# Optimization experiments

Hardware: AMD Instinct MI355X
Metric: run time of the kernel (lower is better)

Reference implementation:

```python
import jax, jax.numpy as jnp
import numpy as np

B, S, H = 4, 4096, 1024
F = 2048          # expert_intermediate_size
E = 8             # num_experts (== num_local_experts, no expert parallelism)
TOPK = 2
INIT_STD = 0.02


def setup_inputs() -> dict:
    key = jax.random.key(0)
    k_hs, k_w, k_e, k_w1, k_w2 = jax.random.split(key, 5)
    hidden_states = jax.random.normal(k_hs, (B, S, H), dtype=jnp.float32)
    expert_weights = jax.random.uniform(k_w, (B * S, TOPK), dtype=jnp.float32)
    top_experts = jax.random.randint(k_e, (B * S, TOPK), 0, E).astype(jnp.int64)
    w1 = INIT_STD * jax.random.normal(k_w1, (E, H, F), dtype=jnp.float32)
    w2 = INIT_STD * jax.random.normal(k_w2, (E, F, H), dtype=jnp.float32)
    b1 = jnp.zeros((E, F), dtype=jnp.float32)
    b2 = jnp.zeros((E, H), dtype=jnp.float32)
    return {"hidden_states": hidden_states, "expert_weights": expert_weights,
            "top_experts": top_experts, "w1": w1, "b1": b1, "w2": w2, "b2": b2}


def reference(hidden_states, expert_weights, top_experts, w1, b1, w2, b2):
    # Equivalent math to megablocks-style gather -> grouped GEMM -> weighted scatter,
    # expressed as masked per-expert GEMMs (sort/permute is a pure reordering and
    # cancels out in the scatter-with-weights combine).
    b, s, h = hidden_states.shape
    x = hidden_states.reshape(-1, h)                       # [T, H]
    T = x.shape[0]
    topk = top_experts.shape[-1]
    fe = top_experts.reshape(-1)                           # [T*topk] routed expert ids
    fw = expert_weights.reshape(-1)                        # [T*topk] routing weights
    xr = jnp.repeat(x, topk, axis=0)                       # [T*topk, H] (gather w/ topk replication)
    out = jnp.zeros_like(xr)
    n_experts = w1.shape[0]
    for e in range(n_experts):                             # small fixed expert loop
        he = jax.nn.gelu(xr @ w1[e] + b1[e], approximate=False) @ w2[e] + b2[e]
        out = out + jnp.where((fe == e)[:, None], he, 0.0)
    # scatter back with routing weights: weighted sum over topk per token
    y = (fw[:, None] * out).reshape(T, topk, h).sum(axis=1)
    return y.reshape(b, s, h)
```

## Files before the change

### kernel.cpp

```cpp
#include <hip/hip_runtime.h>
#include <hip/hip_bf16.h>
#include <math.h>

#define TOKENS 16384
#define HD 1024
#define FD 2048
#define NEXP 8
#define RP_MAX (264 * 128)
#define MAX_MT 264
#define NTN1 16
#define NTN2 8

#define NB_CONV 2048
#define NB_W1   1024
#define NB_W2   1024
#define NB_PREP (NB_CONV + NB_W1 + NB_W2 + 1)

typedef __bf16 bf16x8 __attribute__((ext_vector_type(8)));
typedef float f32x4 __attribute__((ext_vector_type(4)));
typedef unsigned short u16;
typedef unsigned int u32;
typedef unsigned long long u64;

__device__ __forceinline__ u16 f2bf(float f) {
    union { float f; u32 u; } v; v.f = f;
    return (u16)((v.u + 0x7FFFu + ((v.u >> 16) & 1u)) >> 16);
}

__device__ __forceinline__ u32 pk_bf16(float lo, float hi) {
    u32 p;
    asm("v_cvt_pk_bf16_f32 %0, %1, %2" : "=v"(p) : "v"(lo), "v"(hi));
    return p;
}

__device__ __forceinline__ float gelu_f(float v) {
    float u = __builtin_fmaf(0.044715f * v * v, v, v);
    float ez = __builtin_amdgcn_exp2f(-2.302208f * u);
    return v * __builtin_amdgcn_rcpf(1.0f + ez);
}

#define GLOAD16(g, l) __builtin_amdgcn_global_load_lds( \
    (const __attribute__((address_space(1))) u32*)(g),  \
    (__attribute__((address_space(3))) u32*)(l), 16, 0, 0)

__global__ __launch_bounds__(1024) void mega_prep(
    const float* __restrict__ x, u16* __restrict__ xb,
    const float* __restrict__ w1, u16* __restrict__ w1t,
    const float* __restrict__ w2, u16* __restrict__ w2t,
    const int* __restrict__ te,
    int* sorted_rid, int* inv, int* tileE, int* tileRow,
    int* numTiles, int* padcum)
{
    __shared__ __align__(16) char ldsT[32768];
    __shared__ int cntS[NEXP], offsS[NEXP], fillS[NEXP], padS[NEXP], ntS;
    int b = blockIdx.x;
    int tid = threadIdx.x;

    if (b < NB_CONV) {
        int i = b * 1024 + tid;
        const float4* xv = (const float4*)x;
        float4 a = xv[i * 2], c = xv[i * 2 + 1];
        union { u16 s[8]; uint4 v; } o;
        o.s[0] = f2bf(a.x); o.s[1] = f2bf(a.y); o.s[2] = f2bf(a.z); o.s[3] = f2bf(a.w);
        o.s[4] = f2bf(c.x); o.s[5] = f2bf(c.y); o.s[6] = f2bf(c.z); o.s[7] = f2bf(c.w);
        *(uint4*)(xb + (size_t)i * 8) = o.v;
        return;
    }
    if (b < NB_CONV + NB_W1 + NB_W2) {
        const float* src; u16* dst; int K, N, n0, k0, e;
        if (b < NB_CONV + NB_W1) {
            int bb = b - NB_CONV;
            e = bb >> 7; int r = bb & 127;
            n0 = (r & 15) * 128; k0 = (r >> 4) * 128;
            K = HD; N = FD; src = w1; dst = w1t;
        } else {
            int bb = b - NB_CONV - NB_W1;
            e = bb >> 7; int r = bb & 127;
            n0 = (r & 7) * 128; k0 = (r >> 3) * 128;
            K = FD; N = HD; src = w2; dst = w2t;
        }
        const float* s = src + (size_t)e * K * N + (size_t)k0 * N + n0;
        u16* d = dst + (size_t)e * N * K + (size_t)n0 * K + k0;
        int tx = tid & 31, ty = tid >> 5;
        #pragma unroll
        for (int p = 0; p < 4; p++) {
            int k = p * 32 + ty;
            float4 v = *(const float4*)(s + (size_t)k * N + tx * 4);
            union { u16 q[4]; u64 u; } o;
            o.q[0] = f2bf(v.x); o.q[1] = f2bf(v.y); o.q[2] = f2bf(v.z); o.q[3] = f2bf(v.w);
            int phys = tx ^ (k & 31);
            *(u64*)(ldsT + k * 256 + phys * 8) = o.u;
        }
        __syncthreads();
        int tx2 = tid & 15, ty2 = tid >> 4;
        #pragma unroll
        for (int p = 0; p < 2; p++) {
            int n = p * 64 + ty2;
            union { u16 q[8]; uint4 u; } o;
            #pragma unroll
            for (int j = 0; j < 8; j++) {
                int k = tx2 * 8 + j;
                int phys = (n >> 2) ^ (k & 31);
                o.q[j] = *(const u16*)(ldsT + k * 256 + phys * 8 + (n & 3) * 2);
            }
            *(uint4*)(d + (size_t)n * K + tx2 * 8) = o.u;
        }
        return;
    }

    int lane = tid & 63;
    if (tid < NEXP) cntS[tid] = 0;
    __syncthreads();
    int h[NEXP] = {0, 0, 0, 0, 0, 0, 0, 0};
    for (int j = tid; j < TOKENS * 2; j += 1024) {
        int v = te[j];
        #pragma unroll
        for (int e = 0; e < NEXP; e++) h[e] += (v == e);
    }
    #pragma unroll
    for (int e = 0; e < NEXP; e++) {
        int s = h[e];
        #pragma unroll
        for (int o = 32; o > 0; o >>= 1) s += __shfl_down(s, o, 64);
        if (lane == 0 && s) atomicAdd(&cntS[e], s);
    }
    __syncthreads();
    if (tid == 0) {
        int o = 0, t = 0, pc = 0;
        for (int e = 0; e < NEXP; e++) {
            offsS[e] = o; fillS[e] = 0;
            int pad = o - pc;
            padS[e] = pad; padcum[e] = pad;
            int c = cntS[e];
            int nt = (c + 127) >> 7;
            for (int i = 0; i < nt; i++) { tileE[t] = e; tileRow[t] = o + i * 128; t++; }
            o += nt * 128; pc += c;
        }
        ntS = t;
        *numTiles = t;
    }
    __syncthreads();
    int tot = ntS * 128;
    for (int i = tid; i < tot; i += 1024) sorted_rid[i] = -1;
    __syncthreads();
    for (int j = tid; j < TOKENS * 2; j += 1024) {
        int v = te[j];
        int base = 0;
        #pragma unroll
        for (int e = 0; e < NEXP; e++) {
            unsigned long long m = __ballot(v == e);
            if (m) {
                int ldr = (int)__builtin_ctzll(m);
                int bb = 0;
                if (lane == ldr) bb = atomicAdd(&fillS[e], __popcll(m));
                bb = __shfl(bb, ldr, 64);
                if (v == e) base = bb + (int)__popcll(m & ((1ull << lane) - 1ull));
            }
        }
        int p = offsS[v] + base;
        sorted_rid[p] = j;
        inv[j] = p - padS[v];
    }
}



__global__ __launch_bounds__(256, 2) void gemm1_kernel(
    const u16* __restrict__ Xb, const u16* __restrict__ W1t,
    const float* __restrict__ b1, const int* __restrict__ sorted_rid,
    const int* __restrict__ tileE, const int* __restrict__ tileRow,
    const int* __restrict__ numTiles, u16* __restrict__ Hact)
{
    int bid = blockIdx.x;
    int xcd = bid & 7, slot = bid >> 3;
    int mt = xcd + (slot / NTN1) * 8;
    int n0 = (slot % NTN1) * 128;
    if (mt >= *numTiles) return;
    int e = tileE[mt];
    int row0 = tileRow[mt];

    __shared__ __align__(16) u16 As[128 * 64];
    __shared__ __align__(16) u16 Bs[128 * 64];

    int tid = threadIdx.x;
    int wave = tid >> 6, lane = tid & 63;
    int laneR = lane & 15, kgrp = lane >> 4;

    const u16* gA[4]; const u16* gB[4];
    #pragma unroll
    for (int i = 0; i < 4; i++) {
        int c = i * 256 + tid;
        int r = c >> 3, kc = c & 7;
        int kcs = kc ^ (r & 7);
        int rid = sorted_rid[row0 + r];
        int tok = rid < 0 ? 0 : (rid >> 1);
        gA[i] = Xb + (size_t)tok * HD + kcs * 8;
        gB[i] = W1t + ((size_t)e * FD + (n0 + r)) * HD + kcs * 8;
    }
    char* AsB = (char*)As; char* BsB = (char*)Bs;

    f32x4 acc[4][4] = {};

    int wr = wave >> 1, wc = wave & 1;
    int off0 = ((kgrp ^ (lane & 7)) << 4);
    int off1 = off0 ^ 64;
    const char* Abase = AsB + (wr * 64 + laneR) * 128;
    const char* Bbase = BsB + (wc * 64 + laneR) * 128;

    for (int kt = 0; kt < HD / 64; kt++) {
        #pragma unroll
        for (int i = 0; i < 4; i++)
            GLOAD16(gA[i], AsB + i * 4096 + wave * 1024);
        #pragma unroll
        for (int i = 0; i < 4; i++)
            GLOAD16(gB[i], BsB + i * 4096 + wave * 1024);
        #pragma unroll
        for (int i = 0; i < 4; i++) { gA[i] += 64; gB[i] += 64; }
        __syncthreads();
        #pragma unroll
        for (int kk = 0; kk < 2; kk++) {
            int off = kk ? off1 : off0;
            bf16x8 a[4], b[4];
            #pragma unroll
            for (int m = 0; m < 4; m++) a[m] = *(const bf16x8*)(Abase + m * 2048 + off);
            #pragma unroll
            for (int n = 0; n < 4; n++) b[n] = *(const bf16x8*)(Bbase + n * 2048 + off);
            #pragma unroll
            for (int m = 0; m < 4; m++)
                #pragma unroll
                for (int n = 0; n < 4; n++)
                    acc[m][n] = __builtin_amdgcn_mfma_f32_16x16x32_bf16(b[n], a[m], acc[m][n], 0, 0, 0);
        }
        __syncthreads();
    }

    const float* b1e = b1 + e * FD + n0;
    #pragma unroll
    for (int mf = 0; mf < 4; mf++) {
        int grow = row0 + wr * 64 + mf * 16 + laneR;
        u16* hrow = Hact + (size_t)grow * FD + n0;
        #pragma unroll
        for (int nf = 0; nf < 4; nf++) {
            int c = wc * 64 + nf * 16 + kgrp * 4;
            float4 bb = *(const float4*)(b1e + c);
            float g0 = gelu_f(acc[mf][nf][0] + bb.x);
            float g1 = gelu_f(acc[mf][nf][1] + bb.y);
            float g2 = gelu_f(acc[mf][nf][2] + bb.z);
            float g3 = gelu_f(acc[mf][nf][3] + bb.w);
            uint2 p = make_uint2(pk_bf16(g0, g1), pk_bf16(g2, g3));
            *(uint2*)(hrow + c) = p;
        }
    }
}


__global__ __launch_bounds__(256, 2) void gemm2_kernel(
    const u16* __restrict__ Hact, const u16* __restrict__ W2t,
    const float* __restrict__ b2, const int* __restrict__ sorted_rid,
    const int* __restrict__ padcum,
    const int* __restrict__ tileE, const int* __restrict__ tileRow,
    const int* __restrict__ numTiles, u16* __restrict__ Out2)
{
    int bid = blockIdx.x;
    int xcd = bid & 7, slot = bid >> 3;
    int mt = xcd + (slot / NTN2) * 8;
    int n0 = (slot % NTN2) * 128;
    if (mt >= *numTiles) return;
    int e = tileE[mt];
    int row0 = tileRow[mt];

    __shared__ __align__(16) u16 As[128 * 64];
    __shared__ __align__(16) u16 Bs[128 * 64];

    int tid = threadIdx.x;
    int wave = tid >> 6, lane = tid & 63;
    int laneR = lane & 15, kgrp = lane >> 4;

    const u16* gA[4]; const u16* gB[4];
    #pragma unroll
    for (int i = 0; i < 4; i++) {
        int c = i * 256 + tid;
        int r = c >> 3, kc = c & 7;
        int kcs = kc ^ (r & 7);
        gA[i] = Hact + (size_t)(row0 + r) * FD + kcs * 8;
        gB[i] = W2t + ((size_t)e * HD + (n0 + r)) * FD + kcs * 8;
    }
    char* AsB = (char*)As; char* BsB = (char*)Bs;

    f32x4 acc[4][4] = {};

    int wr = wave >> 1, wc = wave & 1;
    int off0 = ((kgrp ^ (lane & 7)) << 4);
    int off1 = off0 ^ 64;
    const char* Abase = AsB + (wr * 64 + laneR) * 128;
    const char* Bbase = BsB + (wc * 64 + laneR) * 128;

    for (int kt = 0; kt < FD / 64; kt++) {
        #pragma unroll
        for (int i = 0; i < 4; i++)
            GLOAD16(gA[i], AsB + i * 4096 + wave * 1024);
        #pragma unroll
        for (int i = 0; i < 4; i++)
            GLOAD16(gB[i], BsB + i * 4096 + wave * 1024);
        #pragma unroll
        for (int i = 0; i < 4; i++) { gA[i] += 64; gB[i] += 64; }
        __syncthreads();
        #pragma unroll
        for (int kk = 0; kk < 2; kk++) {
            int off = kk ? off1 : off0;
            bf16x8 a[4], b[4];
            #pragma unroll
            for (int m = 0; m < 4; m++) a[m] = *(const bf16x8*)(Abase + m * 2048 + off);
            #pragma unroll
            for (int n = 0; n < 4; n++) b[n] = *(const bf16x8*)(Bbase + n * 2048 + off);
            #pragma unroll
            for (int m = 0; m < 4; m++)
                #pragma unroll
                for (int n = 0; n < 4; n++)
                    acc[m][n] = __builtin_amdgcn_mfma_f32_16x16x32_bf16(b[n], a[m], acc[m][n], 0, 0, 0);
        }
        __syncthreads();
    }

    const float* b2e = b2 + e * HD + n0;
    int pc = padcum[e];
    #pragma unroll
    for (int mf = 0; mf < 4; mf++) {
        int rr = row0 + wr * 64 + mf * 16 + laneR;
        int rid = sorted_rid[rr];
        if (rid < 0) continue;
        u16* orow = Out2 + (size_t)(rr - pc) * HD + n0;
        #pragma unroll
        for (int nf = 0; nf < 4; nf++) {
            int c = wc * 64 + nf * 16 + kgrp * 4;
            float4 bb = *(const float4*)(b2e + c);
            float v0 = acc[mf][nf][0] + bb.x;
            float v1 = acc[mf][nf][1] + bb.y;
            float v2 = acc[mf][nf][2] + bb.z;
            float v3 = acc[mf][nf][3] + bb.w;
            uint2 p = make_uint2(pk_bf16(v0, v1), pk_bf16(v2, v3));
            *(uint2*)(orow + c) = p;
        }
    }
}


__global__ void combine_kernel(const u16* __restrict__ Out2, const int* __restrict__ inv,
                               const float* __restrict__ ew, float* __restrict__ y) {
    int i = blockIdx.x * blockDim.x + threadIdx.x;
    int tok = i >> 7;
    int c0 = (i & 127) << 3;
    int s0 = inv[2 * tok], s1 = inv[2 * tok + 1];
    float w0 = ew[2 * tok], w1 = ew[2 * tok + 1];
    union { uint4 v; u16 s[8]; } a, b;
    a.v = *(const uint4*)(Out2 + (size_t)s0 * HD + c0);
    b.v = *(const uint4*)(Out2 + (size_t)s1 * HD + c0);
    float out[8];
    #pragma unroll
    for (int j = 0; j < 8; j++) {
        union { u32 u; float f; } fa, fb;
        fa.u = (u32)a.s[j] << 16;
        fb.u = (u32)b.s[j] << 16;
        out[j] = w0 * fa.f + w1 * fb.f;
    }
    float4* yp = (float4*)(y + (size_t)tok * HD + c0);
    yp[0] = *(const float4*)&out[0];
    yp[1] = *(const float4*)&out[4];
}


extern "C" void kernel_launch(void* const* d_in, const int* in_sizes, int n_in,
                              void* d_out, int out_size, void* d_ws, size_t ws_size,
                              hipStream_t stream) {
    const float* x  = (const float*)d_in[0];
    const float* ew = (const float*)d_in[1];
    const int*   te = (const int*)d_in[2];
    const float* w1 = (const float*)d_in[3];
    const float* b1 = (const float*)d_in[4];
    const float* w2 = (const float*)d_in[5];
    const float* b2 = (const float*)d_in[6];
    float* y = (float*)d_out;

    char* ws = (char*)d_ws;
    u16* Xb   = (u16*)(ws);
    u16* W1t  = (u16*)(ws + 33554432);
    u16* Out2 = (u16*)(ws);
    u16* W2t  = (u16*)(ws + 67108864);
    u16* Hact = (u16*)(ws + 100663296);
    char* ip  = ws + 239075328;
    int* numTiles = (int*)(ip);
    int* padcum   = (int*)(ip + 64);
    int* tileE    = (int*)(ip + 128);
    int* tileRow  = (int*)(ip + 2048);
    int* sorted   = (int*)(ip + 4096);
    int* inv      = (int*)(ip + 139264);

    mega_prep<<<NB_PREP, 1024, 0, stream>>>(
        x, Xb, w1, W1t, w2, W2t, te, sorted, inv, tileE, tileRow, numTiles, padcum);

    gemm1_kernel<<<MAX_MT * NTN1, 256, 0, stream>>>(
        Xb, W1t, b1, sorted, tileE, tileRow, numTiles, Hact);

    gemm2_kernel<<<MAX_MT * NTN2, 256, 0, stream>>>(
        Hact, W2t, b2, sorted, padcum, tileE, tileRow, numTiles, Out2);

    combine_kernel<<<(TOKENS * 128) / 256, 256, 0, stream>>>(Out2, inv, ew, y);
}
```

Before: 445.5 us.

## Move W2 conversion into gemm1 tail blocks and start routing block first

The fp32-to-bf16 transpose of w2 moves out of the prep kernel and into 1024 extra blocks appended to the gemm1 grid, where it can fill idle slots while the GEMM runs. The single-block routing/sort work moves to block 0 of the prep kernel so it is scheduled first rather than last, shortening the prep kernel's critical tail. The transpose blocks use 256 threads instead of 1024, and gemm1's shared buffers become one array so the transpose can reuse them. The risk is that the extra blocks compete with gemm1 tiles for CU occupancy and memory bandwidth.

After: 446.4 us. Within noise of the previous version (+0.2%).

```diff
diff --git a/kernel.cpp b/kernel.cpp
--- a/kernel.cpp
+++ b/kernel.cpp
@@ -13,8 +13,10 @@
 
 #define NB_CONV 2048
 #define NB_W1   1024
-#define NB_W2   1024
-#define NB_PREP (NB_CONV + NB_W1 + NB_W2 + 1)
+#define NB_PREP (1 + NB_CONV + NB_W1)
+
+#define G1_BLOCKS (MAX_MT * NTN1)
+#define NB_W2     1024
 
 typedef __bf16 bf16x8 __attribute__((ext_vector_type(8)));
 typedef float f32x4 __attribute__((ext_vector_type(4)));
@@ -46,7 +48,6 @@
 __global__ __launch_bounds__(1024) void mega_prep(
     const float* __restrict__ x, u16* __restrict__ xb,
     const float* __restrict__ w1, u16* __restrict__ w1t,
-    const float* __restrict__ w2, u16* __restrict__ w2t,
     const int* __restrict__ te,
     int* sorted_rid, int* inv, int* tileE, int* tileRow,
     int* numTiles, int* padcum)
@@ -56,8 +57,64 @@
     int b = blockIdx.x;
     int tid = threadIdx.x;
 
-    if (b < NB_CONV) {
-        int i = b * 1024 + tid;
+    if (b == 0) {
+        int lane = tid & 63;
+        if (tid < NEXP) cntS[tid] = 0;
+        __syncthreads();
+        int h[NEXP] = {0, 0, 0, 0, 0, 0, 0, 0};
+        for (int j = tid; j < TOKENS * 2; j += 1024) {
+            int v = te[j];
+            #pragma unroll
+            for (int e = 0; e < NEXP; e++) h[e] += (v == e);
+        }
+        #pragma unroll
+        for (int e = 0; e < NEXP; e++) {
+            int s = h[e];
+            #pragma unroll
+            for (int o = 32; o > 0; o >>= 1) s += __shfl_down(s, o, 64);
+            if (lane == 0 && s) atomicAdd(&cntS[e], s);
+        }
+        __syncthreads();
+        if (tid == 0) {
+            int o = 0, t = 0, pc = 0;
+            for (int e = 0; e < NEXP; e++) {
+                offsS[e] = o; fillS[e] = 0;
+                int pad = o - pc;
+                padS[e] = pad; padcum[e] = pad;
+                int c = cntS[e];
+                int nt = (c + 127) >> 7;
+                for (int i = 0; i < nt; i++) { tileE[t] = e; tileRow[t] = o + i * 128; t++; }
+                o += nt * 128; pc += c;
+            }
+            ntS = t;
+            *numTiles = t;
+        }
+        __syncthreads();
+        int tot = ntS * 128;
+        for (int i = tid; i < tot; i += 1024) sorted_rid[i] = -1;
+        __syncthreads();
+        for (int j = tid; j < TOKENS * 2; j += 1024) {
+            int v = te[j];
+            int base = 0;
+            #pragma unroll
+            for (int e = 0; e < NEXP; e++) {
+                unsigned long long m = __ballot(v == e);
+                if (m) {
+                    int ldr = (int)__builtin_ctzll(m);
+                    int bb = 0;
+                    if (lane == ldr) bb = atomicAdd(&fillS[e], __popcll(m));
+                    bb = __shfl(bb, ldr, 64);
+                    if (v == e) base = bb + (int)__popcll(m & ((1ull << lane) - 1ull));
+                }
+            }
+            int p = offsS[v] + base;
+            sorted_rid[p] = j;
+            inv[j] = p - padS[v];
+        }
+        return;
+    }
+    if (b <= NB_CONV) {
+        int i = (b - 1) * 1024 + tid;
         const float4* xv = (const float4*)x;
         float4 a = xv[i * 2], c = xv[i * 2 + 1];
         union { u16 s[8]; uint4 v; } o;
@@ -66,21 +123,13 @@
         *(uint4*)(xb + (size_t)i * 8) = o.v;
         return;
     }
-    if (b < NB_CONV + NB_W1 + NB_W2) {
-        const float* src; u16* dst; int K, N, n0, k0, e;
-        if (b < NB_CONV + NB_W1) {
-            int bb = b - NB_CONV;
-            e = bb >> 7; int r = bb & 127;
-            n0 = (r & 15) * 128; k0 = (r >> 4) * 128;
-            K = HD; N = FD; src = w1; dst = w1t;
-        } else {
-            int bb = b - NB_CONV - NB_W1;
-            e = bb >> 7; int r = bb & 127;
-            n0 = (r & 7) * 128; k0 = (r >> 3) * 128;
-            K = FD; N = HD; src = w2; dst = w2t;
-        }
-        const float* s = src + (size_t)e * K * N + (size_t)k0 * N + n0;
-        u16* d = dst + (size_t)e * N * K + (size_t)n0 * K + k0;
+    {
+        int bb = b - 1 - NB_CONV;
+        int e = bb >> 7; int r = bb & 127;
+        int n0 = (r & 15) * 128, k0 = (r >> 4) * 128;
+        const int K = HD, N = FD;
+        const float* s = w1 + (size_t)e * K * N + (size_t)k0 * N + n0;
+        u16* d = w1t + (size_t)e * N * K + (size_t)n0 * K + k0;
         int tx = tid & 31, ty = tid >> 5;
         #pragma unroll
         for (int p = 0; p < 4; p++) {
@@ -105,61 +154,6 @@
             }
             *(uint4*)(d + (size_t)n * K + tx2 * 8) = o.u;
         }
-        return;
-    }
-
-    int lane = tid & 63;
-    if (tid < NEXP) cntS[tid] = 0;
-    __syncthreads();
-    int h[NEXP] = {0, 0, 0, 0, 0, 0, 0, 0};
-    for (int j = tid; j < TOKENS * 2; j += 1024) {
-        int v = te[j];
-        #pragma unroll
-        for (int e = 0; e < NEXP; e++) h[e] += (v == e);
-    }
-    #pragma unroll
-    for (int e = 0; e < NEXP; e++) {
-        int s = h[e];
-        #pragma unroll
-        for (int o = 32; o > 0; o >>= 1) s += __shfl_down(s, o, 64);
-        if (lane == 0 && s) atomicAdd(&cntS[e], s);
-    }
-    __syncthreads();
-    if (tid == 0) {
-        int o = 0, t = 0, pc = 0;
-        for (int e = 0; e < NEXP; e++) {
-            offsS[e] = o; fillS[e] = 0;
-            int pad = o - pc;
-            padS[e] = pad; padcum[e] = pad;
-            int c = cntS[e];
-            int nt = (c + 127) >> 7;
-            for (int i = 0; i < nt; i++) { tileE[t] = e; tileRow[t] = o + i * 128; t++; }
-            o += nt * 128; pc += c;
-        }
-        ntS = t;
-        *numTiles = t;
-    }
-    __syncthreads();
-    int tot = ntS * 128;
-    for (int i = tid; i < tot; i += 1024) sorted_rid[i] = -1;
-    __syncthreads();
-    for (int j = tid; j < TOKENS * 2; j += 1024) {
-        int v = te[j];
-        int base = 0;
-        #pragma unroll
-        for (int e = 0; e < NEXP; e++) {
-            unsigned long long m = __ballot(v == e);
-            if (m) {
-                int ldr = (int)__builtin_ctzll(m);
-                int bb = 0;
-                if (lane == ldr) bb = atomicAdd(&fillS[e], __popcll(m));
-                bb = __shfl(bb, ldr, 64);
-                if (v == e) base = bb + (int)__popcll(m & ((1ull << lane) - 1ull));
-            }
-        }
-        int p = offsS[v] + base;
-        sorted_rid[p] = j;
-        inv[j] = p - padS[v];
     }
 }
 
@@ -169,9 +163,48 @@
     const u16* __restrict__ Xb, const u16* __restrict__ W1t,
     const float* __restrict__ b1, const int* __restrict__ sorted_rid,
     const int* __restrict__ tileE, const int* __restrict__ tileRow,
-    const int* __restrict__ numTiles, u16* __restrict__ Hact)
+    const int* __restrict__ numTiles, u16* __restrict__ Hact,
+    const float* __restrict__ w2, u16* __restrict__ w2t)
 {
+    __shared__ __align__(16) u16 SMEM[2 * 128 * 64];
+    int tid = threadIdx.x;
     int bid = blockIdx.x;
+
+    if (bid >= G1_BLOCKS) {
+        char* ldsT = (char*)SMEM;
+        int bb = bid - G1_BLOCKS;
+        int e = bb >> 7; int r = bb & 127;
+        int n0 = (r & 7) * 128, k0 = (r >> 3) * 128;
+        const int K = FD, N = HD;
+        const float* s = w2 + (size_t)e * K * N + (size_t)k0 * N + n0;
+        u16* d = w2t + (size_t)e * N * K + (size_t)n0 * K + k0;
+        #pragma unroll
+        for (int p = 0; p < 16; p++) {
+            int idx = p * 256 + tid;
+            int k = idx >> 5, tx = idx & 31;
+            float4 v = *(const float4*)(s + (size_t)k * N + tx * 4);
+            union { u16 q[4]; u64 u; } o;
+            o.q[0] = f2bf(v.x); o.q[1] = f2bf(v.y); o.q[2] = f2bf(v.z); o.q[3] = f2bf(v.w);
+            int phys = tx ^ (k & 31);
+            *(u64*)(ldsT + k * 256 + phys * 8) = o.u;
+        }
+        __syncthreads();
+        #pragma unroll
+        for (int p = 0; p < 8; p++) {
+            int idx = p * 256 + tid;
+            int n = idx >> 4, tx2 = idx & 15;
+            union { u16 q[8]; uint4 u; } o;
+            #pragma unroll
+            for (int j = 0; j < 8; j++) {
+                int k = tx2 * 8 + j;
+                int phys = (n >> 2) ^ (k & 31);
+                o.q[j] = *(const u16*)(ldsT + k * 256 + phys * 8 + (n & 3) * 2);
+            }
+            *(uint4*)(d + (size_t)n * K + tx2 * 8) = o.u;
+        }
+        return;
+    }
+
     int xcd = bid & 7, slot = bid >> 3;
     int mt = xcd + (slot / NTN1) * 8;
     int n0 = (slot % NTN1) * 128;
@@ -179,10 +212,6 @@
     int e = tileE[mt];
     int row0 = tileRow[mt];
 
-    __shared__ __align__(16) u16 As[128 * 64];
-    __shared__ __align__(16) u16 Bs[128 * 64];
-
-    int tid = threadIdx.x;
     int wave = tid >> 6, lane = tid & 63;
     int laneR = lane & 15, kgrp = lane >> 4;
 
@@ -197,7 +226,8 @@
         gA[i] = Xb + (size_t)tok * HD + kcs * 8;
         gB[i] = W1t + ((size_t)e * FD + (n0 + r)) * HD + kcs * 8;
     }
-    char* AsB = (char*)As; char* BsB = (char*)Bs;
+    char* AsB = (char*)SMEM;
+    char* BsB = (char*)(SMEM + 128 * 64);
 
     f32x4 acc[4][4] = {};
 
@@ -396,10 +426,10 @@
     int* inv      = (int*)(ip + 139264);
 
     mega_prep<<<NB_PREP, 1024, 0, stream>>>(
-        x, Xb, w1, W1t, w2, W2t, te, sorted, inv, tileE, tileRow, numTiles, padcum);
-
-    gemm1_kernel<<<MAX_MT * NTN1, 256, 0, stream>>>(
-        Xb, W1t, b1, sorted, tileE, tileRow, numTiles, Hact);
+        x, Xb, w1, W1t, te, sorted, inv, tileE, tileRow, numTiles, padcum);
+
+    gemm1_kernel<<<G1_BLOCKS + NB_W2, 256, 0, stream>>>(
+        Xb, W1t, b1, sorted, tileE, tileRow, numTiles, Hact, w2, W2t);
 
     gemm2_kernel<<<MAX_MT * NTN2, 256, 0, stream>>>(
         Hact, W2t, b2, sorted, padcum, tileE, tileRow, numTiles, Out2);
```

## Move routing block first in prep and group GEMM tiles for L2 reuse

Applied to the files above, without the earlier changes.

The serial routing/sort block in the prep kernel moves from the last block index to block 0, so it is scheduled first and overlaps with the conversion blocks instead of trailing them. The GEMM block-to-tile mapping now groups four M tiles together across the N tiles within each XCD, aiming for better weight/activation reuse in cache. Grid sizes are recomputed as 8*9*4*NTN, which gives 288 M tiles against the earlier 264 and so adds some blocks that exit early.

New measurement: 429.0 us. 1.04x faster.

```diff
diff --git a/kernel.cpp b/kernel.cpp
--- a/kernel.cpp
+++ b/kernel.cpp
@@ -8,13 +8,17 @@
 #define NEXP 8
 #define RP_MAX (264 * 128)
 #define MAX_MT 264
+#define MTL_MAX 33
+#define QG 9
 #define NTN1 16
 #define NTN2 8
+#define G1_BLOCKS (8 * QG * 4 * NTN1)
+#define G2_BLOCKS (8 * QG * 4 * NTN2)
 
 #define NB_CONV 2048
 #define NB_W1   1024
 #define NB_W2   1024
-#define NB_PREP (NB_CONV + NB_W1 + NB_W2 + 1)
+#define NB_PREP (1 + NB_CONV + NB_W1 + NB_W2)
 
 typedef __bf16 bf16x8 __attribute__((ext_vector_type(8)));
 typedef float f32x4 __attribute__((ext_vector_type(4)));
@@ -56,8 +60,64 @@
     int b = blockIdx.x;
     int tid = threadIdx.x;
 
-    if (b < NB_CONV) {
-        int i = b * 1024 + tid;
+    if (b == 0) {
+        int lane = tid & 63;
+        if (tid < NEXP) cntS[tid] = 0;
+        __syncthreads();
+        int h[NEXP] = {0, 0, 0, 0, 0, 0, 0, 0};
+        for (int j = tid; j < TOKENS * 2; j += 1024) {
+            int v = te[j];
+            #pragma unroll
+            for (int e = 0; e < NEXP; e++) h[e] += (v == e);
+        }
+        #pragma unroll
+        for (int e = 0; e < NEXP; e++) {
+            int s = h[e];
+            #pragma unroll
+            for (int o = 32; o > 0; o >>= 1) s += __shfl_down(s, o, 64);
+            if (lane == 0 && s) atomicAdd(&cntS[e], s);
+        }
+        __syncthreads();
+        if (tid == 0) {
+            int o = 0, t = 0, pc = 0;
+            for (int e = 0; e < NEXP; e++) {
+                offsS[e] = o; fillS[e] = 0;
+                int pad = o - pc;
+                padS[e] = pad; padcum[e] = pad;
+                int c = cntS[e];
+                int nt = (c + 127) >> 7;
+                for (int i = 0; i < nt; i++) { tileE[t] = e; tileRow[t] = o + i * 128; t++; }
+                o += nt * 128; pc += c;
+            }
+            ntS = t;
+            *numTiles = t;
+        }
+        __syncthreads();
+        int tot = ntS * 128;
+        for (int i = tid; i < tot; i += 1024) sorted_rid[i] = -1;
+        __syncthreads();
+        for (int j = tid; j < TOKENS * 2; j += 1024) {
+            int v = te[j];
+            int base = 0;
+            #pragma unroll
+            for (int e = 0; e < NEXP; e++) {
+                unsigned long long m = __ballot(v == e);
+                if (m) {
+                    int ldr = (int)__builtin_ctzll(m);
+                    int bb = 0;
+                    if (lane == ldr) bb = atomicAdd(&fillS[e], __popcll(m));
+                    bb = __shfl(bb, ldr, 64);
+                    if (v == e) base = bb + (int)__popcll(m & ((1ull << lane) - 1ull));
+                }
+            }
+            int p = offsS[v] + base;
+            sorted_rid[p] = j;
+            inv[j] = p - padS[v];
+        }
+        return;
+    }
+    if (b <= NB_CONV) {
+        int i = (b - 1) * 1024 + tid;
         const float4* xv = (const float4*)x;
         float4 a = xv[i * 2], c = xv[i * 2 + 1];
         union { u16 s[8]; uint4 v; } o;
@@ -66,15 +126,15 @@
         *(uint4*)(xb + (size_t)i * 8) = o.v;
         return;
     }
-    if (b < NB_CONV + NB_W1 + NB_W2) {
+    {
         const float* src; u16* dst; int K, N, n0, k0, e;
-        if (b < NB_CONV + NB_W1) {
-            int bb = b - NB_CONV;
+        if (b <= NB_CONV + NB_W1) {
+            int bb = b - 1 - NB_CONV;
             e = bb >> 7; int r = bb & 127;
             n0 = (r & 15) * 128; k0 = (r >> 4) * 128;
             K = HD; N = FD; src = w1; dst = w1t;
         } else {
-            int bb = b - NB_CONV - NB_W1;
+            int bb = b - 1 - NB_CONV - NB_W1;
             e = bb >> 7; int r = bb & 127;
             n0 = (r & 7) * 128; k0 = (r >> 3) * 128;
             K = FD; N = HD; src = w2; dst = w2t;
@@ -105,61 +165,6 @@
             }
             *(uint4*)(d + (size_t)n * K + tx2 * 8) = o.u;
         }
-        return;
-    }
-
-    int lane = tid & 63;
-    if (tid < NEXP) cntS[tid] = 0;
-    __syncthreads();
-    int h[NEXP] = {0, 0, 0, 0, 0, 0, 0, 0};
-    for (int j = tid; j < TOKENS * 2; j += 1024) {
-        int v = te[j];
-        #pragma unroll
-        for (int e = 0; e < NEXP; e++) h[e] += (v == e);
-    }
-    #pragma unroll
-    for (int e = 0; e < NEXP; e++) {
-        int s = h[e];
-        #pragma unroll
-        for (int o = 32; o > 0; o >>= 1) s += __shfl_down(s, o, 64);
-        if (lane == 0 && s) atomicAdd(&cntS[e], s);
-    }
-    __syncthreads();
-    if (tid == 0) {
-        int o = 0, t = 0, pc = 0;
-        for (int e = 0; e < NEXP; e++) {
-            offsS[e] = o; fillS[e] = 0;
-            int pad = o - pc;
-            padS[e] = pad; padcum[e] = pad;
-            int c = cntS[e];
-            int nt = (c + 127) >> 7;
-            for (int i = 0; i < nt; i++) { tileE[t] = e; tileRow[t] = o + i * 128; t++; }
-            o += nt * 128; pc += c;
-        }
-        ntS = t;
-        *numTiles = t;
-    }
-    __syncthreads();
-    int tot = ntS * 128;
-    for (int i = tid; i < tot; i += 1024) sorted_rid[i] = -1;
-    __syncthreads();
-    for (int j = tid; j < TOKENS * 2; j += 1024) {
-        int v = te[j];
-        int base = 0;
-        #pragma unroll
-        for (int e = 0; e < NEXP; e++) {
-            unsigned long long m = __ballot(v == e);
-            if (m) {
-                int ldr = (int)__builtin_ctzll(m);
-                int bb = 0;
-                if (lane == ldr) bb = atomicAdd(&fillS[e], __popcll(m));
-                bb = __shfl(bb, ldr, 64);
-                if (v == e) base = bb + (int)__popcll(m & ((1ull << lane) - 1ull));
-            }
-        }
-        int p = offsS[v] + base;
-        sorted_rid[p] = j;
-        inv[j] = p - padS[v];
     }
 }
 
@@ -173,8 +178,10 @@
 {
     int bid = blockIdx.x;
     int xcd = bid & 7, slot = bid >> 3;
-    int mt = xcd + (slot / NTN1) * 8;
-    int n0 = (slot % NTN1) * 128;
+    int grp = slot >> 6, rem = slot & 63;
+    int mtl = grp * 4 + (rem & 3);
+    int n0 = (rem >> 2) * 128;
+    int mt = xcd + mtl * 8;
     if (mt >= *numTiles) return;
     int e = tileE[mt];
     int row0 = tileRow[mt];
@@ -263,8 +270,10 @@
 {
     int bid = blockIdx.x;
     int xcd = bid & 7, slot = bid >> 3;
-    int mt = xcd + (slot / NTN2) * 8;
-    int n0 = (slot % NTN2) * 128;
+    int grp = slot >> 5, rem = slot & 31;
+    int mtl = grp * 4 + (rem & 3);
+    int n0 = (rem >> 2) * 128;
+    int mt = xcd + mtl * 8;
     if (mt >= *numTiles) return;
     int e = tileE[mt];
     int row0 = tileRow[mt];
@@ -398,10 +407,10 @@
     mega_prep<<<NB_PREP, 1024, 0, stream>>>(
         x, Xb, w1, W1t, w2, W2t, te, sorted, inv, tileE, tileRow, numTiles, padcum);
 
-    gemm1_kernel<<<MAX_MT * NTN1, 256, 0, stream>>>(
+    gemm1_kernel<<<G1_BLOCKS, 256, 0, stream>>>(
         Xb, W1t, b1, sorted, tileE, tileRow, numTiles, Hact);
 
-    gemm2_kernel<<<MAX_MT * NTN2, 256, 0, stream>>>(
+    gemm2_kernel<<<G2_BLOCKS, 256, 0, stream>>>(
         Hact, W2t, b2, sorted, padcum, tileE, tileRow, numTiles, Out2);
 
     combine_kernel<<<(TOKENS * 128) / 256, 256, 0, stream>>>(Out2, inv, ew, y);
```
